# Kernel optimization log

Hardware: AMD Instinct MI355X
Metric: run time of the kernel (lower is better)

Reference implementation:

```python
import jax, jax.numpy as jnp
import numpy as np

D_MODEL = 1024
NHEAD = 16
HEAD_DIM = D_MODEL // NHEAD
DFF = 4096
EPS = 1e-5


def _layer_norm(x, gamma, beta):
    mu = jnp.mean(x, axis=-1, keepdims=True)
    var = jnp.mean(jnp.square(x - mu), axis=-1, keepdims=True)
    return (x - mu) * jax.lax.rsqrt(var + EPS) * gamma + beta


def setup_inputs() -> dict:
    key = jax.random.key(0)
    ks = jax.random.split(key, 16)
    s = 1.0 / np.sqrt(D_MODEL)
    sf = 1.0 / np.sqrt(DFF)
    inp = {
        "x": jax.random.normal(ks[0], (4, 4096, D_MODEL), dtype=jnp.float32),
        "wq": jax.random.uniform(ks[1], (D_MODEL, D_MODEL), jnp.float32, -s, s),
        "bq": jnp.zeros((D_MODEL,), jnp.float32),
        "wk": jax.random.uniform(ks[2], (D_MODEL, D_MODEL), jnp.float32, -s, s),
        "bk": jnp.zeros((D_MODEL,), jnp.float32),
        "wv": jax.random.uniform(ks[3], (D_MODEL, D_MODEL), jnp.float32, -s, s),
        "bv": jnp.zeros((D_MODEL,), jnp.float32),
        "wo": jax.random.uniform(ks[4], (D_MODEL, D_MODEL), jnp.float32, -s, s),
        "bo": jnp.zeros((D_MODEL,), jnp.float32),
        "w1": jax.random.uniform(ks[5], (D_MODEL, 2 * DFF), jnp.float32, -s, s),
        "b1": jnp.zeros((2 * DFF,), jnp.float32),
        "w2": jax.random.uniform(ks[6], (DFF, D_MODEL), jnp.float32, -sf, sf),
        "b2": jnp.zeros((D_MODEL,), jnp.float32),
        "g1": jnp.ones((D_MODEL,), jnp.float32),
        "be1": jnp.zeros((D_MODEL,), jnp.float32),
        "g2": jnp.ones((D_MODEL,), jnp.float32),
        "be2": jnp.zeros((D_MODEL,), jnp.float32),
    }
    return inp


def reference(x, wq, bq, wk, bk, wv, bv, wo, bo, w1, b1, w2, b2, g1, be1, g2, be2):
    B, S, _ = x.shape
    # --- sublayer 1: pre-norm + linear attention ---
    h = _layer_norm(x, g1, be1)
    q = (h @ wq + bq).reshape(B, S, NHEAD, HEAD_DIM).transpose(0, 2, 1, 3)
    k = (h @ wk + bk).reshape(B, S, NHEAD, HEAD_DIM).transpose(0, 2, 1, 3)
    v = (h @ wv + bv).reshape(B, S, NHEAD, HEAD_DIM).transpose(0, 2, 1, 3)
    q = jax.nn.elu(q) + 1.0
    k = jax.nn.elu(k) + 1.0
    # kv: [B,H,d,e] = sum_s k[...,s,d] v[...,s,e]  (O(n) linear attention)
    kv = jnp.einsum("bhsd,bhse->bhde", k, v)
    attn = jnp.einsum("bhsd,bhde->bhse", q, kv)
    attn = attn.transpose(0, 2, 1, 3).reshape(B, S, D_MODEL)
    x = x + (attn @ wo + bo)
    # --- sublayer 2: pre-norm + GEGLU FFN ---
    h = _layer_norm(x, g2, be2)
    ff = h @ w1 + b1
    g, lin = ff[..., :DFF], ff[..., DFF:]
    ff = jax.nn.gelu(g, approximate=False) * lin
    x = x + (ff @ w2 + b2)
    return x
```

## Files before the change

kernel.cpp:

```cpp
#include <hip/hip_runtime.h>

typedef unsigned short u16;
typedef u16  u16x2  __attribute__((ext_vector_type(2)));
typedef u16  u16x4  __attribute__((ext_vector_type(4)));
typedef u16  u16x8  __attribute__((ext_vector_type(8)));
typedef float f32x4 __attribute__((ext_vector_type(4)));
typedef __bf16 bf16x8 __attribute__((ext_vector_type(8)));

#define D_MODEL 1024
#define DFF     4096
#define SEQ     4096
#define BATCH   4
#define NHEAD   16
#define MROWS   (BATCH*SEQ)
#define MCHUNK  4096

#define BM 128
#define BN 128
#define BK 32

__device__ __forceinline__ float bf2f(u16 u) {
  unsigned v = ((unsigned)u) << 16;
  return __builtin_bit_cast(float, v);
}
__device__ __forceinline__ u16 f2bf(float f) {
  unsigned u = __builtin_bit_cast(unsigned, f);
  u += 0x7fffu + ((u >> 16) & 1u);
  return (u16)(u >> 16);
}

__device__ __forceinline__ void gload16(void* lds, const void* g) {
  __builtin_amdgcn_global_load_lds(
      (const __attribute__((address_space(1))) unsigned*)g,
      (__attribute__((address_space(3))) unsigned*)lds, 16, 0, 0);
}

__device__ __forceinline__ int xcd_swz_bid() {
  const int gx = gridDim.x;
  const int nwg = gx * gridDim.y;
  int bid = blockIdx.y * gx + blockIdx.x;
  const int cpx = nwg >> 3;
  return (bid & 7) * cpx + (bid >> 3);
}

__global__ __launch_bounds__(256)
void transpose_kernel(const float* __restrict__ W, u16* __restrict__ Wt, int K, int N)
{
  __shared__ u16 tile[32][33];
  const int n0 = blockIdx.x * 32, k0 = blockIdx.y * 32;
  const int tx = threadIdx.x & 31, ty = threadIdx.x >> 5;
#pragma unroll
  for (int r = ty; r < 32; r += 8)
    tile[r][tx] = f2bf(W[(size_t)(k0 + r) * N + n0 + tx]);
  __syncthreads();
#pragma unroll
  for (int r = ty; r < 32; r += 8)
    Wt[(size_t)(n0 + r) * K + k0 + tx] = tile[tx][r];
}

template<typename T>
__global__ __launch_bounds__(256)
void ln_kernel(const T* __restrict__ x, const float* __restrict__ g,
               const float* __restrict__ be, u16* __restrict__ out)
{
  const int row = blockIdx.x;
  const int t = threadIdx.x;
  float v0, v1, v2, v3;
  if constexpr (sizeof(T) == 4) {
    f32x4 u = ((const f32x4*)((const float*)x + (size_t)row * D_MODEL))[t];
    v0 = u.x; v1 = u.y; v2 = u.z; v3 = u.w;
  } else {
    u16x4 u = ((const u16x4*)((const u16*)x + (size_t)row * D_MODEL))[t];
    v0 = bf2f(u.x); v1 = bf2f(u.y); v2 = bf2f(u.z); v3 = bf2f(u.w);
  }
  float s  = v0 + v1 + v2 + v3;
  float s2 = v0*v0 + v1*v1 + v2*v2 + v3*v3;
#pragma unroll
  for (int off = 32; off > 0; off >>= 1) {
    s  += __shfl_down(s,  off);
    s2 += __shfl_down(s2, off);
  }
  __shared__ float red[8];
  if ((t & 63) == 0) { red[t >> 6] = s; red[4 + (t >> 6)] = s2; }
  __syncthreads();
  float S  = red[0] + red[1] + red[2] + red[3];
  float S2 = red[4] + red[5] + red[6] + red[7];
  float mu  = S * (1.f / D_MODEL);
  float var = S2 * (1.f / D_MODEL) - mu * mu;
  var = fmaxf(var, 0.f);
  float rs  = rsqrtf(var + 1e-5f);
  f32x4 gu = ((const f32x4*)g)[t];
  f32x4 bu = ((const f32x4*)be)[t];
  u16x4 o;
  o.x = f2bf((v0 - mu) * rs * gu.x + bu.x);
  o.y = f2bf((v1 - mu) * rs * gu.y + bu.y);
  o.z = f2bf((v2 - mu) * rs * gu.z + bu.z);
  o.w = f2bf((v3 - mu) * rs * gu.w + bu.w);
  ((u16x4*)(out + (size_t)row * D_MODEL))[t] = o;
}

template<int MODE>
__global__ __launch_bounds__(256, 2)
void gemm_kernel(const u16* __restrict__ A, const u16* __restrict__ Bt,
                 const float* __restrict__ bias, const void* __restrict__ resv,
                 void* __restrict__ outv, int N, int K)
{
  __shared__ __align__(16) u16 lA[2][BM * BK];
  __shared__ __align__(16) u16 lB[2][BN * BK];
  const float* resf = (const float*)resv;
  const u16*   resb = (const u16*)resv;
  const int tid = threadIdx.x;
  const int wave = tid >> 6, lane = tid & 63;
  const int quad = lane >> 4, ln = lane & 15;
  const int bid = xcd_swz_bid();
  const int bm = (bid / (int)gridDim.x) * BM, bn = (bid % (int)gridDim.x) * BN;
  const int wm = (wave >> 1) * 64, wn = (wave & 1) * 64;

  f32x4 acc[4][4] = {};

  const int c0 = tid,       r0 = c0 >> 2, q0 = c0 & 3;
  const int c1 = tid + 256, r1 = c1 >> 2, q1 = c1 & 3;
  const u16* gA0 = A  + (size_t)(bm + r0) * K + q0 * 8;
  const u16* gA1 = A  + (size_t)(bm + r1) * K + q1 * 8;
  const u16* gB0 = Bt + (size_t)(bn + r0) * K + q0 * 8;
  const u16* gB1 = Bt + (size_t)(bn + r1) * K + q1 * 8;
  const int d0 = wave * 64 * 8;
  const int d1 = (256 + wave * 64) * 8;

  gload16(&lA[0][d0], gA0);
  gload16(&lA[0][d1], gA1);
  gload16(&lB[0][d0], gB0);
  gload16(&lB[0][d1], gB1);
  __syncthreads();

  int cur = 0;
  for (int k0 = 0; k0 < K; k0 += BK) {
    const int nxt = cur ^ 1;
    if (k0 + BK < K) {
      gload16(&lA[nxt][d0], gA0 + k0 + BK);
      gload16(&lA[nxt][d1], gA1 + k0 + BK);
      gload16(&lB[nxt][d0], gB0 + k0 + BK);
      gload16(&lB[nxt][d1], gB1 + k0 + BK);
    }
    bf16x8 af[4], bfr[4];
#pragma unroll
    for (int i = 0; i < 4; ++i) {
      af[i]  = *(const bf16x8*)&lA[cur][(wm + i * 16 + ln) * BK + quad * 8];
      bfr[i] = *(const bf16x8*)&lB[cur][(wn + i * 16 + ln) * BK + quad * 8];
    }
#pragma unroll
    for (int i = 0; i < 4; ++i)
#pragma unroll
      for (int j = 0; j < 4; ++j)
        acc[i][j] = __builtin_amdgcn_mfma_f32_16x16x32_bf16(af[i], bfr[j], acc[i][j], 0, 0, 0);
    __syncthreads();
    cur = nxt;
  }

#pragma unroll
  for (int j = 0; j < 4; ++j) {
    const int col = bn + wn + j * 16 + ln;
    const float bv = bias[col];
#pragma unroll
    for (int i = 0; i < 4; ++i) {
#pragma unroll
      for (int r = 0; r < 4; ++r) {
        const int row = bm + wm + i * 16 + quad * 4 + r;
        const size_t off = (size_t)row * N + col;
        float vv = acc[i][j][r] + bv;
        if (MODE == 1) vv = vv > 0.f ? vv + 1.f : __expf(vv);
        if (MODE == 2) vv += resf[off];
        if (MODE == 3) vv += bf2f(resb[off]);
        if (MODE == 3) ((float*)outv)[off] = vv;
        else           ((u16*)outv)[off]   = f2bf(vv);
      }
    }
  }
}

__global__ __launch_bounds__(256, 2)
void ffn1_kernel(const u16* __restrict__ A, const u16* __restrict__ Wt,
                 const float* __restrict__ b1, u16* __restrict__ out, int K)
{
  __shared__ __align__(16) u16 lA [2][BM * BK];
  __shared__ __align__(16) u16 lBg[2][BN * BK];
  __shared__ __align__(16) u16 lBl[2][BN * BK];
  const int tid = threadIdx.x;
  const int wave = tid >> 6, lane = tid & 63;
  const int quad = lane >> 4, ln = lane & 15;
  const int bid = xcd_swz_bid();
  const int bm = (bid / (int)gridDim.x) * BM, bn = (bid % (int)gridDim.x) * BN;
  const int wm = (wave >> 1) * 64, wn = (wave & 1) * 64;

  f32x4 accg[4][4] = {};
  f32x4 accl[4][4] = {};

  const int c0 = tid,       r0 = c0 >> 2, q0 = c0 & 3;
  const int c1 = tid + 256, r1 = c1 >> 2, q1 = c1 & 3;
  const u16* gA0 = A  + (size_t)(bm + r0) * K + q0 * 8;
  const u16* gA1 = A  + (size_t)(bm + r1) * K + q1 * 8;
  const u16* gG0 = Wt + (size_t)(bn + r0) * K + q0 * 8;
  const u16* gG1 = Wt + (size_t)(bn + r1) * K + q1 * 8;
  const u16* gL0 = Wt + (size_t)(DFF + bn + r0) * K + q0 * 8;
  const u16* gL1 = Wt + (size_t)(DFF + bn + r1) * K + q1 * 8;
  const int d0 = wave * 64 * 8;
  const int d1 = (256 + wave * 64) * 8;

  gload16(&lA [0][d0], gA0);
  gload16(&lA [0][d1], gA1);
  gload16(&lBg[0][d0], gG0);
  gload16(&lBg[0][d1], gG1);
  gload16(&lBl[0][d0], gL0);
  gload16(&lBl[0][d1], gL1);
  __syncthreads();

  int cur = 0;
  for (int k0 = 0; k0 < K; k0 += BK) {
    const int nxt = cur ^ 1;
    if (k0 + BK < K) {
      gload16(&lA [nxt][d0], gA0 + k0 + BK);
      gload16(&lA [nxt][d1], gA1 + k0 + BK);
      gload16(&lBg[nxt][d0], gG0 + k0 + BK);
      gload16(&lBg[nxt][d1], gG1 + k0 + BK);
      gload16(&lBl[nxt][d0], gL0 + k0 + BK);
      gload16(&lBl[nxt][d1], gL1 + k0 + BK);
    }
    bf16x8 af[4], bg[4], bl[4];
#pragma unroll
    for (int i = 0; i < 4; ++i) {
      af[i] = *(const bf16x8*)&lA [cur][(wm + i * 16 + ln) * BK + quad * 8];
      bg[i] = *(const bf16x8*)&lBg[cur][(wn + i * 16 + ln) * BK + quad * 8];
      bl[i] = *(const bf16x8*)&lBl[cur][(wn + i * 16 + ln) * BK + quad * 8];
    }
#pragma unroll
    for (int i = 0; i < 4; ++i)
#pragma unroll
      for (int j = 0; j < 4; ++j) {
        accg[i][j] = __builtin_amdgcn_mfma_f32_16x16x32_bf16(af[i], bg[j], accg[i][j], 0, 0, 0);
        accl[i][j] = __builtin_amdgcn_mfma_f32_16x16x32_bf16(af[i], bl[j], accl[i][j], 0, 0, 0);
      }
    __syncthreads();
    cur = nxt;
  }

#pragma unroll
  for (int j = 0; j < 4; ++j) {
    const int col = bn + wn + j * 16 + ln;
    const float bgv = b1[col];
    const float blv = b1[DFF + col];
#pragma unroll
    for (int i = 0; i < 4; ++i) {
#pragma unroll
      for (int r = 0; r < 4; ++r) {
        const int row = bm + wm + i * 16 + quad * 4 + r;
        float gg = accg[i][j][r] + bgv;
        float ll = accl[i][j][r] + blv;
        float ge = 0.5f * gg * (1.f + erff(gg * 0.70710678118f));
        out[(size_t)row * DFF + col] = f2bf(ge * ll);
      }
    }
  }
}

#define KVCH 1024
__global__ __launch_bounds__(256)
void kvmm_kernel(const u16* __restrict__ kk, const u16* __restrict__ vv,
                 float* __restrict__ kvpart)
{
  __shared__ __align__(16) u16 lK[32][66];
  __shared__ __align__(16) u16 lV[32][66];
  const int blk = blockIdx.x;
  const int c = blk & 3, bh = blk >> 2;
  const int b = bh >> 4, h = bh & 15;
  const int tid = threadIdx.x, wave = tid >> 6, lane = tid & 63;
  const int quad = lane >> 4, ln = lane & 15;
  const int dbase = (wave >> 1) * 32, ebase = (wave & 1) * 32;
  f32x4 acc[2][2] = {};

  const int srow = tid >> 3;
  const int dcol = (tid & 7) * 8;
  const size_t gbase = ((size_t)b * SEQ + (size_t)c * KVCH + srow) * D_MODEL + h * 64 + dcol;
  const u16* gk = kk + gbase;
  const u16* gv = vv + gbase;

  for (int s0 = 0; s0 < KVCH; s0 += 32) {
    u16x8 k8 = *(const u16x8*)(gk + (size_t)s0 * D_MODEL);
    u16x8 v8 = *(const u16x8*)(gv + (size_t)s0 * D_MODEL);
    __syncthreads();
    u16x2* wk2 = (u16x2*)&lK[srow][dcol];
    u16x2* wv2 = (u16x2*)&lV[srow][dcol];
#pragma unroll
    for (int p = 0; p < 4; ++p) {
      u16x2 a; a.x = k8[2*p]; a.y = k8[2*p+1]; wk2[p] = a;
      u16x2 w; w.x = v8[2*p]; w.y = v8[2*p+1]; wv2[p] = w;
    }
    __syncthreads();
    bf16x8 af[2], bf[2];
#pragma unroll
    for (int i = 0; i < 2; ++i) {
      const int dd = dbase + i * 16 + ln;
      const int ee = ebase + i * 16 + ln;
      u16x8 at, bt;
#pragma unroll
      for (int j = 0; j < 8; ++j) {
        at[j] = lK[quad * 8 + j][dd];
        bt[j] = lV[quad * 8 + j][ee];
      }
      af[i] = __builtin_bit_cast(bf16x8, at);
      bf[i] = __builtin_bit_cast(bf16x8, bt);
    }
#pragma unroll
    for (int i = 0; i < 2; ++i)
#pragma unroll
      for (int j = 0; j < 2; ++j)
        acc[i][j] = __builtin_amdgcn_mfma_f32_16x16x32_bf16(af[i], bf[j], acc[i][j], 0, 0, 0);
  }

  float* op = kvpart + ((size_t)c * 64 + bh) * 4096;
#pragma unroll
  for (int i = 0; i < 2; ++i)
#pragma unroll
    for (int j = 0; j < 2; ++j)
#pragma unroll
      for (int r = 0; r < 4; ++r) {
        const int d = dbase + i * 16 + quad * 4 + r;
        const int e = ebase + j * 16 + ln;
        op[d * 64 + e] = acc[i][j][r];
      }
}

__global__ __launch_bounds__(256)
void kvreduce_kernel(float* __restrict__ p)
{
  const int i = blockIdx.x * 256 + threadIdx.x;
  f32x4* p4 = (f32x4*)p;
  f32x4 a = p4[i];
  f32x4 b = p4[i + 65536];
  f32x4 c = p4[i + 131072];
  f32x4 d = p4[i + 196608];
  p4[i] = (a + b) + (c + d);
}

__global__ __launch_bounds__(256)
void attn_kernel(const u16* __restrict__ qq, const float* __restrict__ kv,
                 u16* __restrict__ out)
{
  __shared__ __align__(16) float kvs[64 * 64];
  const int blk = blockIdx.x;
  const int sc = blk & 63;
  const int bh = blk >> 6;
  const int b = bh >> 4, h = bh & 15;
  const int t = threadIdx.x;
  const f32x4* src = (const f32x4*)(kv + (size_t)bh * 4096);
  for (int i = t; i < 1024; i += 256) ((f32x4*)kvs)[i] = src[i];
  __syncthreads();
  const int sl = t >> 2, e0 = (t & 3) * 16;
  const size_t row = (size_t)b * SEQ + sc * 64 + sl;
  const u16* qp = qq + row * D_MODEL + h * 64;
  float qv[64];
#pragma unroll
  for (int i = 0; i < 16; ++i) {
    u16x4 u = ((const u16x4*)qp)[i];
    qv[i*4+0] = bf2f(u.x); qv[i*4+1] = bf2f(u.y);
    qv[i*4+2] = bf2f(u.z); qv[i*4+3] = bf2f(u.w);
  }
  f32x4 acc[4] = {};
  for (int d = 0; d < 64; ++d) {
    const float qd = qv[d];
    const f32x4* kr = (const f32x4*)(kvs + d * 64 + e0);
#pragma unroll
    for (int i = 0; i < 4; ++i) acc[i] += qd * kr[i];
  }
  u16* op = out + row * D_MODEL + h * 64 + e0;
#pragma unroll
  for (int i = 0; i < 4; ++i) {
    u16x4 o;
    o.x = f2bf(acc[i][0]); o.y = f2bf(acc[i][1]);
    o.z = f2bf(acc[i][2]); o.w = f2bf(acc[i][3]);
    ((u16x4*)op)[i] = o;
  }
}

extern "C" void kernel_launch(void* const* d_in, const int* in_sizes, int n_in,
                              void* d_out, int out_size, void* d_ws, size_t ws_size,
                              hipStream_t stream)
{
  const float* x   = (const float*)d_in[0];
  const float* wq  = (const float*)d_in[1];
  const float* bq  = (const float*)d_in[2];
  const float* wk  = (const float*)d_in[3];
  const float* bk  = (const float*)d_in[4];
  const float* wv  = (const float*)d_in[5];
  const float* bv  = (const float*)d_in[6];
  const float* wo  = (const float*)d_in[7];
  const float* bo  = (const float*)d_in[8];
  const float* w1  = (const float*)d_in[9];
  const float* b1  = (const float*)d_in[10];
  const float* w2  = (const float*)d_in[11];
  const float* b2  = (const float*)d_in[12];
  const float* g1  = (const float*)d_in[13];
  const float* be1 = (const float*)d_in[14];
  const float* g2  = (const float*)d_in[15];
  const float* be2 = (const float*)d_in[16];

  char* ws = (char*)d_ws;
  const size_t MB = 1024ull * 1024ull;
  u16* wqt = (u16*)(ws + 0 * MB);
  u16* wkt = (u16*)(ws + 2 * MB);
  u16* wvt = (u16*)(ws + 4 * MB);
  u16* wot = (u16*)(ws + 6 * MB);
  u16* w1t = (u16*)(ws + 8 * MB);
  u16* w2t = (u16*)(ws + 24 * MB);

  u16* hb    = (u16*)(ws + 32 * MB);
  u16* x1b   = (u16*)(ws + 32 * MB);
  u16* kb    = (u16*)(ws + 64 * MB);
  u16* qb    = (u16*)(ws + 64 * MB);
  u16* hb2   = (u16*)(ws + 64 * MB);
  u16* vb    = (u16*)(ws + 96 * MB);
  u16* attnb = (u16*)(ws + 96 * MB);
  u16* gbuf  = (u16*)(ws + 96 * MB);
  float* kvpart = (float*)(ws + 2 * MB);

  transpose_kernel<<<dim3(32, 32), 256, 0, stream>>>(wq, wqt, 1024, 1024);
  transpose_kernel<<<dim3(32, 32), 256, 0, stream>>>(wk, wkt, 1024, 1024);
  transpose_kernel<<<dim3(32, 32), 256, 0, stream>>>(wv, wvt, 1024, 1024);
  transpose_kernel<<<dim3(32, 32), 256, 0, stream>>>(wo, wot, 1024, 1024);
  transpose_kernel<<<dim3(256, 32), 256, 0, stream>>>(w1, w1t, 1024, 8192);
  transpose_kernel<<<dim3(32, 128), 256, 0, stream>>>(w2, w2t, 4096, 1024);

  ln_kernel<float><<<MROWS, 256, 0, stream>>>(x, g1, be1, hb);

  dim3 gproj(D_MODEL / BN, MROWS / BM);
  gemm_kernel<1><<<gproj, 256, 0, stream>>>(hb, wkt, bk, nullptr, kb, D_MODEL, D_MODEL);
  gemm_kernel<0><<<gproj, 256, 0, stream>>>(hb, wvt, bv, nullptr, vb, D_MODEL, D_MODEL);

  kvmm_kernel<<<64 * 4, 256, 0, stream>>>(kb, vb, kvpart);
  kvreduce_kernel<<<256, 256, 0, stream>>>(kvpart);

  gemm_kernel<1><<<gproj, 256, 0, stream>>>(hb, wqt, bq, nullptr, qb, D_MODEL, D_MODEL);

  attn_kernel<<<BATCH * NHEAD * (SEQ / 64), 256, 0, stream>>>(qb, kvpart, attnb);

  gemm_kernel<2><<<gproj, 256, 0, stream>>>(attnb, wot, bo, x, x1b, D_MODEL, D_MODEL);

  ln_kernel<u16><<<MROWS, 256, 0, stream>>>(x1b, g2, be2, hb2);

  for (int c = 0; c < MROWS / MCHUNK; ++c) {
    const size_t ro = (size_t)c * MCHUNK;
    ffn1_kernel<<<dim3(DFF / BN, MCHUNK / BM), 256, 0, stream>>>(
        hb2 + ro * D_MODEL, w1t, b1, gbuf, D_MODEL);
    gemm_kernel<3><<<dim3(D_MODEL / BN, MCHUNK / BM), 256, 0, stream>>>(
        gbuf, w2t, b2, x1b + ro * D_MODEL, (float*)d_out + ro * D_MODEL, D_MODEL, DFF);
  }
}
```

Measured before the change: 1.145 ms.

## Triple-buffer GEMM LDS pipeline with explicit vmcnt waits and raw barriers

The generic GEMM moves from a double-buffered to a triple-buffered LDS pipeline that issues loads two k-steps ahead. It waits with explicit s_waitcnt vmcnt counts, so only the oldest tile must land before the barrier, instead of draining all outstanding loads at each __syncthreads. The FFN1 kernel keeps two buffers but uses the same partial vmcnt wait plus raw-barrier scheme, and drops the XCD block swizzle for plain blockIdx mapping. The extra buffer raises LDS use from 32KB to 48KB per block in the GEMM, which may limit the two-blocks-per-CU occupancy. Removing the swizzle may also change L2 locality across XCDs.

```diff
diff --git a/kernel.cpp b/kernel.cpp
--- a/kernel.cpp
+++ b/kernel.cpp
@@ -34,6 +34,13 @@
       (const __attribute__((address_space(1))) unsigned*)g,
       (__attribute__((address_space(3))) unsigned*)lds, 16, 0, 0);
 }
+
+__device__ __forceinline__ void barrier_raw() {
+  asm volatile("" ::: "memory");
+  __builtin_amdgcn_s_barrier();
+  asm volatile("" ::: "memory");
+}
+#define VMWAIT(n) asm volatile("s_waitcnt vmcnt(" #n ")" ::: "memory")
 
 __device__ __forceinline__ int xcd_swz_bid() {
   const int gx = gridDim.x;
@@ -105,8 +112,8 @@
                  const float* __restrict__ bias, const void* __restrict__ resv,
                  void* __restrict__ outv, int N, int K)
 {
-  __shared__ __align__(16) u16 lA[2][BM * BK];
-  __shared__ __align__(16) u16 lB[2][BN * BK];
+  __shared__ __align__(16) u16 lA[3][BM * BK];
+  __shared__ __align__(16) u16 lB[3][BN * BK];
   const float* resf = (const float*)resv;
   const u16*   resb = (const u16*)resv;
   const int tid = threadIdx.x;
@@ -127,21 +134,32 @@
   const int d0 = wave * 64 * 8;
   const int d1 = (256 + wave * 64) * 8;
 
+  const int nk = K / BK;
   gload16(&lA[0][d0], gA0);
   gload16(&lA[0][d1], gA1);
   gload16(&lB[0][d0], gB0);
   gload16(&lB[0][d1], gB1);
-  __syncthreads();
+  gload16(&lA[1][d0], gA0 + BK);
+  gload16(&lA[1][d1], gA1 + BK);
+  gload16(&lB[1][d0], gB0 + BK);
+  gload16(&lB[1][d1], gB1 + BK);
 
   int cur = 0;
-  for (int k0 = 0; k0 < K; k0 += BK) {
-    const int nxt = cur ^ 1;
-    if (k0 + BK < K) {
-      gload16(&lA[nxt][d0], gA0 + k0 + BK);
-      gload16(&lA[nxt][d1], gA1 + k0 + BK);
-      gload16(&lB[nxt][d0], gB0 + k0 + BK);
-      gload16(&lB[nxt][d1], gB1 + k0 + BK);
-    }
+  for (int t = 0; t < nk; ++t) {
+    if (t + 2 < nk) {
+      int wb = cur + 2; if (wb >= 3) wb -= 3;
+      const size_t ko = (size_t)(t + 2) * BK;
+      gload16(&lA[wb][d0], gA0 + ko);
+      gload16(&lA[wb][d1], gA1 + ko);
+      gload16(&lB[wb][d0], gB0 + ko);
+      gload16(&lB[wb][d1], gB1 + ko);
+      VMWAIT(8);
+    } else if (t + 1 < nk) {
+      VMWAIT(4);
+    } else {
+      VMWAIT(0);
+    }
+    barrier_raw();
     bf16x8 af[4], bfr[4];
 #pragma unroll
     for (int i = 0; i < 4; ++i) {
@@ -153,8 +171,8 @@
 #pragma unroll
       for (int j = 0; j < 4; ++j)
         acc[i][j] = __builtin_amdgcn_mfma_f32_16x16x32_bf16(af[i], bfr[j], acc[i][j], 0, 0, 0);
-    __syncthreads();
-    cur = nxt;
+    barrier_raw();
+    cur = cur + 1; if (cur >= 3) cur = 0;
   }
 
 #pragma unroll
@@ -188,8 +206,7 @@
   const int tid = threadIdx.x;
   const int wave = tid >> 6, lane = tid & 63;
   const int quad = lane >> 4, ln = lane & 15;
-  const int bid = xcd_swz_bid();
-  const int bm = (bid / (int)gridDim.x) * BM, bn = (bid % (int)gridDim.x) * BN;
+  const int bm = blockIdx.y * BM, bn = blockIdx.x * BN;
   const int wm = (wave >> 1) * 64, wn = (wave & 1) * 64;
 
   f32x4 accg[4][4] = {};
@@ -206,25 +223,30 @@
   const int d0 = wave * 64 * 8;
   const int d1 = (256 + wave * 64) * 8;
 
+  const int nk = K / BK;
   gload16(&lA [0][d0], gA0);
   gload16(&lA [0][d1], gA1);
   gload16(&lBg[0][d0], gG0);
   gload16(&lBg[0][d1], gG1);
   gload16(&lBl[0][d0], gL0);
   gload16(&lBl[0][d1], gL1);
-  __syncthreads();
 
   int cur = 0;
-  for (int k0 = 0; k0 < K; k0 += BK) {
-    const int nxt = cur ^ 1;
-    if (k0 + BK < K) {
-      gload16(&lA [nxt][d0], gA0 + k0 + BK);
-      gload16(&lA [nxt][d1], gA1 + k0 + BK);
-      gload16(&lBg[nxt][d0], gG0 + k0 + BK);
-      gload16(&lBg[nxt][d1], gG1 + k0 + BK);
-      gload16(&lBl[nxt][d0], gL0 + k0 + BK);
-      gload16(&lBl[nxt][d1], gL1 + k0 + BK);
-    }
+  for (int t = 0; t < nk; ++t) {
+    if (t + 1 < nk) {
+      const int nxt = cur ^ 1;
+      const size_t ko = (size_t)(t + 1) * BK;
+      gload16(&lA [nxt][d0], gA0 + ko);
+      gload16(&lA [nxt][d1], gA1 + ko);
+      gload16(&lBg[nxt][d0], gG0 + ko);
+      gload16(&lBg[nxt][d1], gG1 + ko);
+      gload16(&lBl[nxt][d0], gL0 + ko);
+      gload16(&lBl[nxt][d1], gL1 + ko);
+      VMWAIT(6);
+    } else {
+      VMWAIT(0);
+    }
+    barrier_raw();
     bf16x8 af[4], bg[4], bl[4];
 #pragma unroll
     for (int i = 0; i < 4; ++i) {
@@ -239,8 +261,8 @@
         accg[i][j] = __builtin_amdgcn_mfma_f32_16x16x32_bf16(af[i], bg[j], accg[i][j], 0, 0, 0);
         accl[i][j] = __builtin_amdgcn_mfma_f32_16x16x32_bf16(af[i], bl[j], accl[i][j], 0, 0, 0);
       }
-    __syncthreads();
-    cur = nxt;
+    barrier_raw();
+    cur ^= 1;
   }
 
 #pragma unroll
```

Result: faster. 1.115 ms (-2.7%).
